# Kernel tuning notes

Hardware: AMD Instinct MI355X
Metric: run time of the kernel (lower is better)

The kernel has to match this reference:

```python
import jax, jax.numpy as jnp
import numpy as np

D_MODEL = 1024
N_HEAD = 16
HEAD_DIM = D_MODEL // N_HEAD


def rope_cos_sin(L, head_dim):
    inv_freq = 1.0 / (10000.0 ** (jnp.arange(0, head_dim, 2, dtype=jnp.float32) / head_dim))
    t = jnp.arange(L, dtype=jnp.float32)
    freqs = jnp.einsum('l,d->ld', t, inv_freq)            # (L, head_dim/2)
    emb = jnp.concatenate([freqs, freqs], axis=-1)         # (L, head_dim)
    return jnp.cos(emb), jnp.sin(emb)


def rotate_half(x):
    d = x.shape[-1] // 2
    return jnp.concatenate([-x[..., d:], x[..., :d]], axis=-1)


def setup_inputs() -> dict:
    key = jax.random.key(0)
    ks = jax.random.split(key, 6)
    B, L = 4, 2048
    s_in = 1.0 / np.sqrt(D_MODEL)
    x = jax.random.normal(ks[0], (B, L, D_MODEL), dtype=jnp.float32)
    pad_mask = jnp.zeros((B, L), dtype=bool)
    W_qkv = jax.random.uniform(ks[1], (D_MODEL, 3 * D_MODEL), jnp.float32, -s_in, s_in)
    b_qkv = jax.random.uniform(ks[2], (3 * D_MODEL,), jnp.float32, -s_in, s_in)
    W_out = jax.random.uniform(ks[3], (D_MODEL, D_MODEL), jnp.float32, -s_in, s_in)
    b_out = jax.random.uniform(ks[4], (D_MODEL,), jnp.float32, -s_in, s_in)
    return {"x": x, "pad_mask": pad_mask, "W_qkv": W_qkv, "b_qkv": b_qkv,
            "W_out": W_out, "b_out": b_out}


def reference(x, pad_mask, W_qkv, b_qkv, W_out, b_out):
    B, L, C = x.shape
    H, Dh = N_HEAD, HEAD_DIM
    qkv = x @ W_qkv + b_qkv                                # (B, L, 3C)
    q, k, v = jnp.split(qkv, 3, axis=-1)
    q = q.reshape(B, L, H, Dh).transpose(0, 2, 1, 3)       # (B, H, L, Dh)
    k = k.reshape(B, L, H, Dh).transpose(0, 2, 1, 3)
    v = v.reshape(B, L, H, Dh).transpose(0, 2, 1, 3)
    cos, sin = rope_cos_sin(L, Dh)                         # (L, Dh)
    q = q * cos + rotate_half(q) * sin
    k = k * cos + rotate_half(k) * sin
    att = jnp.einsum('bhqd,bhkd->bhqk', q, k) / jnp.sqrt(jnp.float32(Dh))
    causal = jnp.triu(jnp.ones((L, L), dtype=bool), k=1)   # True above diagonal
    neg_inf = jnp.float32(-jnp.inf)
    att = jnp.where(causal[None, None, :, :], neg_inf, att)
    att = jnp.where(pad_mask[:, None, None, :], neg_inf, att)
    att = jax.nn.softmax(att, axis=-1)
    y = jnp.einsum('bhqk,bhkd->bhqd', att, v)              # (B, H, L, Dh)
    y = y.transpose(0, 2, 1, 3).reshape(B, L, C)
    return y @ W_out + b_out
```

## Files before the change

### kernel.cpp

```cpp
#include <hip/hip_runtime.h>
#include <hip/hip_bf16.h>

typedef __bf16 bf16x8 __attribute__((ext_vector_type(8)));
typedef float f32x4 __attribute__((ext_vector_type(4)));
typedef unsigned short u16x8 __attribute__((ext_vector_type(8)));
typedef unsigned short u16x4 __attribute__((ext_vector_type(4)));

using bf16 = __hip_bfloat16;

#define DEV static __device__ __forceinline__

constexpr int Lq = 2048;

DEV void stage16(const void* g, void* lds_base_uniform, int lane) {
#if __has_builtin(__builtin_amdgcn_global_load_lds)
  (void)lane;
  __builtin_amdgcn_global_load_lds((__attribute__((address_space(1))) void*)g,
                                   (__attribute__((address_space(3))) void*)lds_base_uniform,
                                   16, 0, 0);
#else
  *(u16x8*)((char*)lds_base_uniform + lane * 16) = *(const u16x8*)g;
#endif
}

#if __has_builtin(__builtin_amdgcn_exp2f)
#define EXP2(x) __builtin_amdgcn_exp2f(x)
#else
#define EXP2(x) __exp2f(x)
#endif

DEV unsigned short f2bfbits(float x) {
  bf16 h = __float2bfloat16(x);
  return *(unsigned short*)&h;
}

DEV unsigned f2bf_pk(float lo, float hi) {
  unsigned ul = __builtin_bit_cast(unsigned, lo) + 0x8000u;
  unsigned uh = __builtin_bit_cast(unsigned, hi) + 0x8000u;
  return __builtin_amdgcn_perm(uh, ul, 0x07060302u);
}

DEV f32x4 MFMA16(bf16x8 a, bf16x8 b, f32x4 c) {
  return __builtin_amdgcn_mfma_f32_16x16x32_bf16(a, b, c, 0, 0, 0);
}


__global__ void k_convert_x(const float* __restrict__ x, bf16* __restrict__ xb) {
  size_t i = (size_t)blockIdx.x * 256 + threadIdx.x;
  float4 v = ((const float4*)x)[i];
  size_t o = i * 4;
  xb[o + 0] = __float2bfloat16(v.x);
  xb[o + 1] = __float2bfloat16(v.y);
  xb[o + 2] = __float2bfloat16(v.z);
  xb[o + 3] = __float2bfloat16(v.w);
}

__global__ void k_transpose_w(const float* __restrict__ W, bf16* __restrict__ Wt,
                              int Kd, int Nd) {
  __shared__ bf16 T[32][33];
  const int k0 = blockIdx.x * 32;
  const int n0 = blockIdx.y * 32;
  const int t = threadIdx.x;
  const int cn = t & 31, rk = t >> 5;
#pragma unroll
  for (int p = 0; p < 4; ++p) {
    int k = rk + p * 8;
    T[k][cn] = __float2bfloat16(W[(size_t)(k0 + k) * Nd + n0 + cn]);
  }
  __syncthreads();
#pragma unroll
  for (int p = 0; p < 4; ++p) {
    int n = rk + p * 8;
    Wt[(size_t)(n0 + n) * Kd + k0 + cn] = T[cn][n];
  }
}

__global__ void k_rope_tab(float* __restrict__ ct, float* __restrict__ st) {
  int idx = blockIdx.x * 256 + threadIdx.x;
  int l = idx >> 5, i = idx & 31;
  float inv = powf(10000.0f, -(float)i * (1.0f / 32.0f));
  float a = (float)l * inv;
  ct[idx] = cosf(a);
  st[idx] = sinf(a);
}

template <int EPI>
__launch_bounds__(256, 2)
__global__ void k_gemm(const bf16* __restrict__ A, const bf16* __restrict__ Bt,
                       const float* __restrict__ bias, int Kd,
                       float* __restrict__ outF,
                       bf16* __restrict__ Qb, bf16* __restrict__ Kb, bf16* __restrict__ Vtb,
                       const float* __restrict__ ct, const float* __restrict__ st) {
  __shared__ bf16 As[2][128 * 32];
  __shared__ bf16 Bs[2][128 * 32];
  const int tid = threadIdx.x;
  const int w = tid >> 6, lane = tid & 63;
  const int quad = lane >> 4, l15 = lane & 15;
  const int lin = blockIdx.y * gridDim.x + blockIdx.x;
  const int cpx = (gridDim.x * gridDim.y) >> 3;
  const int swz = (lin & 7) * cpx + (lin >> 3);
  const int nB = swz % gridDim.x, mB = swz / gridDim.x;
  const int wm = (w & 1) * 64, wn = (w >> 1) * 64;
  const int rowg0 = mB * 128, colg0 = nB * 128;
  const int srow = lane >> 2;
  const int sseg = ((lane & 3) ^ ((lane >> 4) & 3)) * 8;
  const int rsw = (l15 >> 2) & 3;

  f32x4 z4 = {0.f, 0.f, 0.f, 0.f};
  f32x4 acc[4][4];
#pragma unroll
  for (int i = 0; i < 4; ++i)
#pragma unroll
    for (int j = 0; j < 4; ++j) acc[i][j] = z4;

  auto stageAB = [&](int k0, int pb) {
#pragma unroll
    for (int t2 = 0; t2 < 2; ++t2) {
      int r16 = w * 32 + t2 * 16;
      stage16(A + (size_t)(rowg0 + r16 + srow) * Kd + k0 + sseg,
              (char*)&As[pb][0] + r16 * 64, lane);
      stage16(Bt + (size_t)(colg0 + r16 + srow) * Kd + k0 + sseg,
              (char*)&Bs[pb][0] + r16 * 64, lane);
    }
  };

  int pb = 0;
  stageAB(0, 0);
  for (int k0 = 0; k0 < Kd; k0 += 32) {
    __syncthreads();
    if (k0 + 32 < Kd) stageAB(k0 + 32, pb ^ 1);
    const bf16* Asp = &As[pb][0];
    const bf16* Bsp = &Bs[pb][0];
    bf16x8 af[4], bfr[4];
#pragma unroll
    for (int i = 0; i < 4; ++i)
      af[i] = *(const bf16x8*)(Asp + (wm + i * 16 + l15) * 32 + ((quad ^ rsw) << 3));
#pragma unroll
    for (int j = 0; j < 4; ++j)
      bfr[j] = *(const bf16x8*)(Bsp + (wn + j * 16 + l15) * 32 + ((quad ^ rsw) << 3));
#pragma unroll
    for (int i = 0; i < 4; ++i)
#pragma unroll
      for (int j = 0; j < 4; ++j)
        acc[i][j] = __builtin_amdgcn_mfma_f32_16x16x32_bf16(af[i], bfr[j], acc[i][j], 0, 0, 0);
    pb ^= 1;
  }

  float bs0 = bias[colg0 + wn + 0 * 16 + l15];
  float bs1 = bias[colg0 + wn + 1 * 16 + l15];
  float bs2 = bias[colg0 + wn + 2 * 16 + l15];
  float bs3 = bias[colg0 + wn + 3 * 16 + l15];

  if (EPI == 1) {
#pragma unroll
    for (int i = 0; i < 4; ++i)
#pragma unroll
      for (int r = 0; r < 4; ++r) {
        int row = rowg0 + wm + i * 16 + quad * 4 + r;
        float* op = outF + (size_t)row * 1024 + colg0 + wn;
        op[0 * 16 + l15] = acc[i][0][r] + bs0;
        op[1 * 16 + l15] = acc[i][1][r] + bs1;
        op[2 * 16 + l15] = acc[i][2][r] + bs2;
        op[3 * 16 + l15] = acc[i][3][r] + bs3;
      }
  } else {
    const int sel = colg0 / 1024;
    const int cb = (colg0 + wn) & 1023;
    const int h = cb >> 6;
    const float bsv[4] = {bs0, bs1, bs2, bs3};
    if (sel == 2) {
#pragma unroll
      for (int i = 0; i < 4; ++i) {
        int l0 = rowg0 + wm + i * 16 + quad * 4;
        int b = l0 >> 11, l = l0 & 2047;
#pragma unroll
        for (int nt = 0; nt < 4; ++nt) {
          int d = nt * 16 + l15;
          u16x4 pk;
#pragma unroll
          for (int r = 0; r < 4; ++r) pk[r] = f2bfbits(acc[i][nt][r] + bsv[nt]);
          *(u16x4*)(Vtb + ((size_t)(b * 16 + h) * 64 + d) * Lq + l) = pk;
        }
      }
    } else {
      bf16* base = (sel == 0) ? Qb : Kb;
      const float qscale = 0.125f * 1.4426950408889634f;
#pragma unroll
      for (int i = 0; i < 4; ++i)
#pragma unroll
        for (int r = 0; r < 4; ++r) {
          int row = rowg0 + wm + i * 16 + quad * 4 + r;
          int b = row >> 11, l = row & 2047;
          float v0 = acc[i][0][r] + bs0;
          float v1 = acc[i][1][r] + bs1;
          float v2 = acc[i][2][r] + bs2;
          float v3 = acc[i][3][r] + bs3;
          bf16* dst = base + ((size_t)(b * 16 + h) * Lq + l) * 64;
          float cA = ct[l * 32 + l15],      sA = st[l * 32 + l15];
          float cB = ct[l * 32 + 16 + l15], sB = st[l * 32 + 16 + l15];
          float o0 = v0 * cA - v2 * sA;
          float o2 = v2 * cA + v0 * sA;
          float o1 = v1 * cB - v3 * sB;
          float o3 = v3 * cB + v1 * sB;
          if (sel == 0) { o0 *= qscale; o1 *= qscale; o2 *= qscale; o3 *= qscale; }
          dst[0 * 16 + l15] = __float2bfloat16(o0);
          dst[1 * 16 + l15] = __float2bfloat16(o1);
          dst[2 * 16 + l15] = __float2bfloat16(o2);
          dst[3 * 16 + l15] = __float2bfloat16(o3);
        }
    }
  }
}


template <bool DIAG>
DEV void softmax_ctx(f32x4 (&s)[4], f32x4 (&o)[4], float& mi, float& li,
                     int qglob, int key0, int quad, int l15) {
  float mloc = -INFINITY;
#pragma unroll
  for (int nt = 0; nt < 4; ++nt)
#pragma unroll
    for (int r = 0; r < 4; ++r) {
      float v = s[nt][r];
      if (DIAG && (key0 + nt * 16 + quad * 4 + r > qglob)) v = -INFINITY;
      s[nt][r] = v;
      mloc = fmaxf(mloc, v);
    }
  mloc = fmaxf(mloc, __shfl_xor(mloc, 16));
  mloc = fmaxf(mloc, __shfl_xor(mloc, 32));
  if (!__all(mloc <= mi + 8.0f)) {
    float mn = fmaxf(mi, mloc);
    float alpha = EXP2(mi - mn);
    li *= alpha;
    mi = mn;
    float av[4];
#pragma unroll
    for (int r = 0; r < 4; ++r) av[r] = __shfl(alpha, quad * 4 + r);
#pragma unroll
    for (int t = 0; t < 4; ++t)
#pragma unroll
      for (int r = 0; r < 4; ++r) o[t][r] *= av[r];
  }
  float rs = 0.f;
#pragma unroll
  for (int nt = 0; nt < 4; ++nt)
#pragma unroll
    for (int r = 0; r < 4; ++r) {
      float p = EXP2(s[nt][r] - mi);
      s[nt][r] = p;
      rs += p;
    }
  rs += __shfl_xor(rs, 16);
  rs += __shfl_xor(rs, 32);
  li += rs;
}

DEV void packP(const f32x4 (&s)[4], bf16* __restrict__ PsW, int quad, int l15) {
#pragma unroll
  for (int nt = 0; nt < 4; ++nt) {
    int chunk = nt * 2 + (quad >> 1);
    uint2 pk2 = {f2bf_pk(s[nt][0], s[nt][1]), f2bf_pk(s[nt][2], s[nt][3])};
    *(uint2*)(PsW + l15 * 64 + ((chunk ^ (l15 & 7)) << 3) + (quad & 1) * 4) = pk2;
  }
}

DEV void pv(const bf16* __restrict__ VsP, const bf16* __restrict__ PsW,
            f32x4 (&o)[4], int quad, int l15) {
  bf16x8 aP0 = *(const bf16x8*)(PsW + l15 * 64 + ((quad ^ (l15 & 7)) << 3));
  bf16x8 aP1 = *(const bf16x8*)(PsW + l15 * 64 + (((4 + quad) ^ (l15 & 7)) << 3));
  __builtin_amdgcn_s_setprio(1);
#pragma unroll
  for (int t = 0; t < 4; ++t) {
    int R = t * 16 + l15;
    bf16x8 bv0 = *(const bf16x8*)(VsP + R * 64 + ((quad ^ (R & 7)) << 3));
    bf16x8 bv1 = *(const bf16x8*)(VsP + R * 64 + (((4 + quad) ^ (R & 7)) << 3));
    o[t] = MFMA16(aP0, bv0, o[t]);
    o[t] = MFMA16(aP1, bv1, o[t]);
  }
  __builtin_amdgcn_s_setprio(0);
}

template <bool DIAGA>
DEV void tile_both(const bf16* __restrict__ KsP, const bf16* __restrict__ VsP,
                   bf16* __restrict__ PsW,
                   bf16x8 aQB0, bf16x8 aQB1, bf16x8 aQA0, bf16x8 aQA1,
                   f32x4 (&oB)[4], float& miB, float& liB,
                   f32x4 (&oA)[4], float& miA, float& liA,
                   int qglobA, int key0, int quad, int l15) {
  bf16x8 aK0[4], aK1[4];
#pragma unroll
  for (int nt = 0; nt < 4; ++nt) {
    int R = nt * 16 + l15;
    aK0[nt] = *(const bf16x8*)(KsP + R * 64 + ((quad ^ (R & 7)) << 3));
    aK1[nt] = *(const bf16x8*)(KsP + R * 64 + (((4 + quad) ^ (R & 7)) << 3));
  }
  f32x4 z4 = {0.f, 0.f, 0.f, 0.f};
  f32x4 sB[4], sA[4];
  __builtin_amdgcn_s_setprio(1);
#pragma unroll
  for (int nt = 0; nt < 4; ++nt) {
    f32x4 t0 = MFMA16(aK0[nt], aQB0, z4);
    sB[nt] = MFMA16(aK1[nt], aQB1, t0);
  }
#pragma unroll
  for (int nt = 0; nt < 4; ++nt) {
    f32x4 t0 = MFMA16(aK0[nt], aQA0, z4);
    sA[nt] = MFMA16(aK1[nt], aQA1, t0);
  }
  __builtin_amdgcn_s_setprio(0);
  softmax_ctx<false>(sB, oB, miB, liB, 0, key0, quad, l15);
  packP(sB, PsW, quad, l15);
  softmax_ctx<DIAGA>(sA, oA, miA, liA, qglobA, key0, quad, l15);
  pv(VsP, PsW, oB, quad, l15);
  packP(sA, PsW, quad, l15);
  pv(VsP, PsW, oA, quad, l15);
}

template <bool DIAGB>
DEV void tile_one(const bf16* __restrict__ KsP, const bf16* __restrict__ VsP,
                  bf16* __restrict__ PsW,
                  bf16x8 aQB0, bf16x8 aQB1,
                  f32x4 (&oB)[4], float& miB, float& liB,
                  int qglobB, int key0, int quad, int l15) {
  bf16x8 aK0[4], aK1[4];
#pragma unroll
  for (int nt = 0; nt < 4; ++nt) {
    int R = nt * 16 + l15;
    aK0[nt] = *(const bf16x8*)(KsP + R * 64 + ((quad ^ (R & 7)) << 3));
    aK1[nt] = *(const bf16x8*)(KsP + R * 64 + (((4 + quad) ^ (R & 7)) << 3));
  }
  f32x4 z4 = {0.f, 0.f, 0.f, 0.f};
  f32x4 sB[4];
  __builtin_amdgcn_s_setprio(1);
#pragma unroll
  for (int nt = 0; nt < 4; ++nt) {
    f32x4 t0 = MFMA16(aK0[nt], aQB0, z4);
    sB[nt] = MFMA16(aK1[nt], aQB1, t0);
  }
  __builtin_amdgcn_s_setprio(0);
  softmax_ctx<DIAGB>(sB, oB, miB, liB, qglobB, key0, quad, l15);
  packP(sB, PsW, quad, l15);
  pv(VsP, PsW, oB, quad, l15);
}

__launch_bounds__(512, 4)
__global__ void k_attn(const bf16* __restrict__ Qb, const bf16* __restrict__ Kb,
                       const bf16* __restrict__ Vt, bf16* __restrict__ Y) {
  __shared__ bf16 Ks[2][64 * 64];
  __shared__ bf16 Vs[2][64 * 64];
  __shared__ bf16 Ps[8][16 * 64];
  const int tid = threadIdx.x;
  const int w = tid >> 6, lane = tid & 63;
  const int quad = lane >> 4, l15 = lane & 15;
  const int wg = w & 3;
  const int g = w >> 2;
  const int lin = blockIdx.y * 8 + blockIdx.x;
  const int swz = (lin & 7) * 64 + (lin >> 3);
  const int bh = swz >> 3, bx = swz & 7;
  const int qp = 2 * bx + g;
  const int qtA = qp, qtB = 31 - qp;
  const int KT = 32 - 2 * bx;
  const int b = bh >> 4, h = bh & 15;

  const int srow8 = lane >> 3;
  const int sseg = ((lane & 7) ^ srow8) * 8;

  bf16* PsW = &Ps[w][0];

  const bf16* QrowA = Qb + ((size_t)bh * Lq + qtA * 64 + wg * 16 + l15) * 64;
  const bf16* QrowB = Qb + ((size_t)bh * Lq + qtB * 64 + wg * 16 + l15) * 64;
  bf16x8 aQA0 = *(const bf16x8*)(QrowA + quad * 8);
  bf16x8 aQA1 = *(const bf16x8*)(QrowA + 32 + quad * 8);
  bf16x8 aQB0 = *(const bf16x8*)(QrowB + quad * 8);
  bf16x8 aQB1 = *(const bf16x8*)(QrowB + 32 + quad * 8);

  f32x4 z4 = {0.f, 0.f, 0.f, 0.f};
  f32x4 oA[4] = {z4, z4, z4, z4}, oB[4] = {z4, z4, z4, z4};
  float miA = -INFINITY, liA = 0.f, miB = -INFINITY, liB = 0.f;

  auto stageKV = [&](int kt, int pb) {
    int r8 = w * 8;
    stage16(Kb + ((size_t)bh * Lq + kt * 64 + r8 + srow8) * 64 + sseg,
            (char*)&Ks[pb][0] + r8 * 128, lane);
    stage16(Vt + ((size_t)bh * 64 + r8 + srow8) * Lq + kt * 64 + sseg,
            (char*)&Vs[pb][0] + r8 * 128, lane);
  };

  int p = 0;
  stageKV(0, 0);
  const int qglobB = qtB * 64 + wg * 16 + l15;
  const int qglobA = qtA * 64 + wg * 16 + l15;

  for (int kt = 0; kt < KT; ++kt) {
    __syncthreads();
    if (kt + 1 < KT) stageKV(kt + 1, p ^ 1);
    const bf16* KsP = &Ks[p][0];
    const bf16* VsP = &Vs[p][0];
    if (kt < qtA)
      tile_both<false>(KsP, VsP, PsW, aQB0, aQB1, aQA0, aQA1,
                       oB, miB, liB, oA, miA, liA, qglobA, kt * 64, quad, l15);
    else if (kt == qtA)
      tile_both<true>(KsP, VsP, PsW, aQB0, aQB1, aQA0, aQA1,
                      oB, miB, liB, oA, miA, liA, qglobA, kt * 64, quad, l15);
    else if (kt < qtB)
      tile_one<false>(KsP, VsP, PsW, aQB0, aQB1,
                      oB, miB, liB, qglobB, kt * 64, quad, l15);
    else if (kt == qtB)
      tile_one<true>(KsP, VsP, PsW, aQB0, aQB1,
                     oB, miB, liB, qglobB, kt * 64, quad, l15);
    p ^= 1;
  }

  float invB = 1.0f / liB, invA = 1.0f / liA;
#pragma unroll
  for (int r = 0; r < 4; ++r) {
    float ivB = __shfl(invB, quad * 4 + r);
    float ivA = __shfl(invA, quad * 4 + r);
    int lrowB = qtB * 64 + wg * 16 + quad * 4 + r;
    bf16* ypB = Y + ((size_t)b * Lq + lrowB) * 1024 + h * 64;
#pragma unroll
    for (int t = 0; t < 4; ++t)
      ypB[t * 16 + l15] = __float2bfloat16(oB[t][r] * ivB);
    int lrowA = qtA * 64 + wg * 16 + quad * 4 + r;
    bf16* ypA = Y + ((size_t)b * Lq + lrowA) * 1024 + h * 64;
#pragma unroll
    for (int t = 0; t < 4; ++t)
      ypA[t * 16 + l15] = __float2bfloat16(oA[t][r] * ivA);
  }
}

extern "C" void kernel_launch(void* const* d_in, const int* in_sizes, int n_in,
                              void* d_out, int out_size, void* d_ws, size_t ws_size,
                              hipStream_t stream) {
  const float* x     = (const float*)d_in[0];
  const float* W_qkv = (const float*)d_in[2];
  const float* b_qkv = (const float*)d_in[3];
  const float* W_out = (const float*)d_in[4];
  const float* b_out = (const float*)d_in[5];
  float* out = (float*)d_out;

  char* ws = (char*)d_ws;
  bf16*  xb   = (bf16*)(ws);
  bf16*  Wqt  = (bf16*)(ws + 16777216);
  bf16*  Wot  = (bf16*)(ws + 23068672);
  bf16*  Qb   = (bf16*)(ws + 25165824);
  bf16*  Kb   = (bf16*)(ws + 41943040);
  bf16*  Vt   = (bf16*)(ws + 75497472);
  bf16*  Y    = (bf16*)(ws + 92274688);
  float* ct   = (float*)(ws + 109051904);
  float* st   = (float*)(ws + 109314048);

  k_convert_x<<<8192, 256, 0, stream>>>(x, xb);
  k_transpose_w<<<dim3(32, 96), 256, 0, stream>>>(W_qkv, Wqt, 1024, 3072);
  k_transpose_w<<<dim3(32, 32), 256, 0, stream>>>(W_out, Wot, 1024, 1024);
  k_rope_tab<<<256, 256, 0, stream>>>(ct, st);

  k_gemm<0><<<dim3(24, 64), 256, 0, stream>>>(xb, Wqt, b_qkv, 1024,
                                              nullptr, Qb, Kb, Vt, ct, st);
  k_attn<<<dim3(8, 64), 512, 0, stream>>>(Qb, Kb, Vt, Y);
  k_gemm<1><<<dim3(8, 64), 256, 0, stream>>>(Y, Wot, b_out, 1024,
                                             out, nullptr, nullptr, nullptr, nullptr, nullptr);
}
```

Before: 284.3 us.

## Deepen GEMM and attention LDS pipelines to four buffers with prefetch distance two

Both the GEMM and attention kernels move from double-buffered LDS staging to a four-slot ring with loads issued two tiles ahead. A manual vmcnt wait plus a raw s_barrier replaces __syncthreads, so only the oldest outstanding tile must have landed before compute starts. The goal is to hide more global-load latency behind MFMA work. The cost is twice the shared memory, which may lower occupancy (especially in attention at 4 blocks of 512 threads), and the hand-counted vmcnt values are a correctness risk.

```diff
diff --git a/kernel.cpp b/kernel.cpp
--- a/kernel.cpp
+++ b/kernel.cpp
@@ -91,8 +91,8 @@
                        float* __restrict__ outF,
                        bf16* __restrict__ Qb, bf16* __restrict__ Kb, bf16* __restrict__ Vtb,
                        const float* __restrict__ ct, const float* __restrict__ st) {
-  __shared__ bf16 As[2][128 * 32];
-  __shared__ bf16 Bs[2][128 * 32];
+  __shared__ bf16 As[4][128 * 32];
+  __shared__ bf16 Bs[4][128 * 32];
   const int tid = threadIdx.x;
   const int w = tid >> 6, lane = tid & 63;
   const int quad = lane >> 4, l15 = lane & 15;
@@ -113,7 +113,8 @@
 #pragma unroll
     for (int j = 0; j < 4; ++j) acc[i][j] = z4;
 
-  auto stageAB = [&](int k0, int pb) {
+  auto stageAB = [&](int kt, int pb) {
+    int k0 = kt * 32;
 #pragma unroll
     for (int t2 = 0; t2 < 2; ++t2) {
       int r16 = w * 32 + t2 * 16;
@@ -124,13 +125,17 @@
     }
   };
 
-  int pb = 0;
+  const int NT = Kd >> 5;
   stageAB(0, 0);
-  for (int k0 = 0; k0 < Kd; k0 += 32) {
-    __syncthreads();
-    if (k0 + 32 < Kd) stageAB(k0 + 32, pb ^ 1);
-    const bf16* Asp = &As[pb][0];
-    const bf16* Bsp = &Bs[pb][0];
+  stageAB(1, 1);
+  for (int t = 0; t < NT; ++t) {
+    int tp = (t + 2 < NT) ? t + 2 : NT - 1;
+    stageAB(tp, (t + 2) & 3);
+    asm volatile("s_waitcnt vmcnt(8)" ::: "memory");
+    __builtin_amdgcn_s_barrier();
+    __builtin_amdgcn_sched_barrier(0);
+    const bf16* Asp = &As[t & 3][0];
+    const bf16* Bsp = &Bs[t & 3][0];
     bf16x8 af[4], bfr[4];
 #pragma unroll
     for (int i = 0; i < 4; ++i)
@@ -143,8 +148,8 @@
 #pragma unroll
       for (int j = 0; j < 4; ++j)
         acc[i][j] = __builtin_amdgcn_mfma_f32_16x16x32_bf16(af[i], bfr[j], acc[i][j], 0, 0, 0);
-    pb ^= 1;
-  }
+  }
+  asm volatile("s_waitcnt vmcnt(0)" ::: "memory");
 
   float bs0 = bias[colg0 + wn + 0 * 16 + l15];
   float bs1 = bias[colg0 + wn + 1 * 16 + l15];
@@ -346,8 +351,8 @@
 __launch_bounds__(512, 4)
 __global__ void k_attn(const bf16* __restrict__ Qb, const bf16* __restrict__ Kb,
                        const bf16* __restrict__ Vt, bf16* __restrict__ Y) {
-  __shared__ bf16 Ks[2][64 * 64];
-  __shared__ bf16 Vs[2][64 * 64];
+  __shared__ bf16 Ks[4][64 * 64];
+  __shared__ bf16 Vs[4][64 * 64];
   __shared__ bf16 Ps[8][16 * 64];
   const int tid = threadIdx.x;
   const int w = tid >> 6, lane = tid & 63;
@@ -386,16 +391,19 @@
             (char*)&Vs[pb][0] + r8 * 128, lane);
   };
 
-  int p = 0;
-  stageKV(0, 0);
   const int qglobB = qtB * 64 + wg * 16 + l15;
   const int qglobA = qtA * 64 + wg * 16 + l15;
 
+  stageKV(0, 0);
+  stageKV(1, 1);
   for (int kt = 0; kt < KT; ++kt) {
-    __syncthreads();
-    if (kt + 1 < KT) stageKV(kt + 1, p ^ 1);
-    const bf16* KsP = &Ks[p][0];
-    const bf16* VsP = &Vs[p][0];
+    int kp = (kt + 2 < KT) ? kt + 2 : KT - 1;
+    stageKV(kp, (kt + 2) & 3);
+    asm volatile("s_waitcnt vmcnt(4)" ::: "memory");
+    __builtin_amdgcn_s_barrier();
+    __builtin_amdgcn_sched_barrier(0);
+    const bf16* KsP = &Ks[kt & 3][0];
+    const bf16* VsP = &Vs[kt & 3][0];
     if (kt < qtA)
       tile_both<false>(KsP, VsP, PsW, aQB0, aQB1, aQA0, aQA1,
                        oB, miB, liB, oA, miA, liA, qglobA, kt * 64, quad, l15);
@@ -408,8 +416,8 @@
     else if (kt == qtB)
       tile_one<true>(KsP, VsP, PsW, aQB0, aQB1,
                      oB, miB, liB, qglobB, kt * 64, quad, l15);
-    p ^= 1;
-  }
+  }
+  asm volatile("s_waitcnt vmcnt(0)" ::: "memory");
 
   float invB = 1.0f / liB, invA = 1.0f / liA;
 #pragma unroll
```

New measurement: 290.3 us. 1.02x slower.
